# Optimization experiments

Measured on AMD Instinct MI355X. Metric: run time of the kernel, lower is better.

## Reference

```python
import jax, jax.numpy as jnp
import numpy as np

TAU = 0.05
EPS = 1e-12


def _l2_normalize(x):
    # F.normalize(p=2): x / max(||x||, eps)
    n = jnp.sqrt(jnp.sum(x * x, axis=-1, keepdims=True))
    return x / jnp.maximum(n, EPS)


def _masked_lse(sim, mask):
    # logsumexp over axis -1 restricted to mask; rows with empty mask are
    # masked out downstream (has_pos), so we guard the log to stay finite.
    neg_inf = jnp.finfo(sim.dtype).min
    mx = jnp.max(jnp.where(mask, sim, neg_inf), axis=-1)
    mx_safe = jnp.where(mx > neg_inf / 2, mx, 0.0)
    s = jnp.sum(jnp.where(mask, jnp.exp(sim - mx_safe[:, None]), 0.0), axis=-1)
    return mx_safe + jnp.log(jnp.where(s > 0, s, 1.0))


def setup_inputs() -> dict:
    key = jax.random.key(0)
    k1, k2, k3, k4 = jax.random.split(key, 4)
    B, S, D = 64, 128, 256
    return {
        "logits": jax.random.normal(k1, (B, S, D), dtype=jnp.float32),
        "labels": jax.random.normal(k2, (B, S, D), dtype=jnp.float32),
        "pad_mask": jax.random.randint(k3, (B, S), 0, 2, dtype=jnp.int32),
        "ad_idxs": jax.random.randint(k4, (B, S), 0, 500, dtype=jnp.int32),
    }


def reference(logits, labels, pad_mask, ad_idxs):
    B, S, D = logits.shape
    q = _l2_normalize(logits.reshape(B * S, D))
    k = _l2_normalize(labels.reshape(B * S, D))
    valid = pad_mask.reshape(B * S).astype(bool)
    ad = ad_idxs.reshape(B * S)

    sim = jnp.einsum("nd,md->nm", q, k) / TAU          # [N, N]
    pair_valid = valid[None, :] & valid[:, None]
    pos_mask = (ad[None, :] == ad[:, None]) & pair_valid

    pos_lse = _masked_lse(sim, pos_mask)
    all_lse = _masked_lse(sim, pair_valid)
    has_pos = jnp.any(pos_mask, axis=-1)

    loss_per_row = -(pos_lse - all_lse)
    # mean over rows with at least one positive (== loss_per_row[has_pos].mean())
    cnt = jnp.sum(has_pos.astype(sim.dtype))
    loss = jnp.sum(jnp.where(has_pos, loss_per_row, 0.0)) / jnp.maximum(cnt, 1.0)
    return loss
```

## Files before the change

kernel.cpp:

```cpp
#include <hip/hip_runtime.h>
#include <hip/hip_bf16.h>
#include <hip/hip_fp8.h>
#include <math.h>

typedef float f32x4 __attribute__((ext_vector_type(4)));
typedef int   i32x4 __attribute__((ext_vector_type(4)));
typedef int   v8i   __attribute__((ext_vector_type(8)));

constexpr int Nn = 8192;
constexpr int Dd = 256;
constexpr float LOG2E     = 1.4426950408889634f;
constexpr float SIM_SCALE = 20.0f * LOG2E;
constexpr float SIM_BIAS  = -20.0f * LOG2E;
constexpr int   SCALE1    = 0x7F7F7F7F;

typedef __attribute__((address_space(1))) const unsigned int gu32;
typedef __attribute__((address_space(3))) unsigned int lu32;
__device__ __forceinline__ void gload16(const unsigned char* g, unsigned char* l) {
  __builtin_amdgcn_global_load_lds((gu32*)(uintptr_t)g, (lu32*)(uintptr_t)l, 16, 0, 0);
}

__global__ __launch_bounds__(256) void prep_kernel(const float* __restrict__ logits,
                                                   const float* __restrict__ labels,
                                                   const int* __restrict__ pad,
                                                   unsigned char* __restrict__ qb,
                                                   unsigned char* __restrict__ kb,
                                                   float* __restrict__ cbias,
                                                   float* __restrict__ g_all,
                                                   float* __restrict__ g_pos) {
  const int j = blockIdx.x * 256 + threadIdx.x;
  if (j < Nn) {
    cbias[j] = pad[j] ? SIM_BIAS : -1e30f;
    g_all[j] = 0.0f;
    g_pos[j] = 0.0f;
  }

  const int gw   = (blockIdx.x * 256 + threadIdx.x) >> 6;
  const int lane = threadIdx.x & 63;
  const float* src;
  unsigned char* dst;
  int row;
  if (gw < Nn) { src = logits; dst = qb; row = gw; }
  else         { src = labels; dst = kb; row = gw - Nn; }

  const float4 v = *reinterpret_cast<const float4*>(src + (size_t)row * Dd + lane * 4);
  float ss = v.x * v.x + v.y * v.y + v.z * v.z + v.w * v.w;
#pragma unroll
  for (int m = 32; m >= 1; m >>= 1) ss += __shfl_xor(ss, m);
  const float scale = 1.0f / fmaxf(sqrtf(ss), 1e-12f);

  const __hip_fp8_e4m3 e0(v.x * scale);
  const __hip_fp8_e4m3 e1(v.y * scale);
  const __hip_fp8_e4m3 e2(v.z * scale);
  const __hip_fp8_e4m3 e3(v.w * scale);
  const unsigned int packed = (unsigned int)e0.__x |
                              ((unsigned int)e1.__x << 8) |
                              ((unsigned int)e2.__x << 16) |
                              ((unsigned int)e3.__x << 24);
  reinterpret_cast<unsigned int*>(dst + (size_t)row * Dd)[lane] = packed;
}

__global__ __launch_bounds__(256, 2) void gemm_lse_kernel(const unsigned char* __restrict__ qb,
                                                          const unsigned char* __restrict__ kb,
                                                          const float* __restrict__ cbias,
                                                          const int* __restrict__ ad,
                                                          float* __restrict__ g_all,
                                                          float* __restrict__ g_pos) {
  __shared__ unsigned char smem[65536];

  const int tid  = threadIdx.x;
  const int lane = tid & 63;
  const int w    = tid >> 6;
  const int wrow = (w >> 1) * 64;
  const int wcolL = (w & 1) * 64;
  const int lq   = lane & 15;
  const int qd   = lane >> 4;
  const int rowBase = blockIdx.x * 128;
  const int colBase = blockIdx.y * 1024;

  const int srl = lane >> 3;
  const int cg  = (lane & 7) ^ srl;
  const unsigned char* gA0 = qb + (size_t)(rowBase + w * 32 + srl) * Dd + cg * 16;
  const unsigned char* gB0 = kb + (size_t)(colBase + w * 32 + srl) * Dd + cg * 16;

#pragma unroll
  for (int kk = 0; kk < 2; ++kk)
#pragma unroll
    for (int i = 0; i < 4; ++i)
      gload16(gA0 + (size_t)i * 8 * Dd + kk * 128,
              &smem[kk * 16384 + (w * 32 + i * 8) * 128]);
#pragma unroll
  for (int i = 0; i < 4; ++i)
    gload16(gB0 + (size_t)i * 8 * Dd, &smem[32768 + (w * 32 + i * 8) * 128]);

  int rowAd[4][4];
#pragma unroll
  for (int mt = 0; mt < 4; ++mt)
#pragma unroll
    for (int r = 0; r < 4; ++r)
      rowAd[mt][r] = ad[rowBase + wrow + mt * 16 + qd * 4 + r];

  float apA[4][4], apP[4][4];
  f32x4 c[4][4];
#pragma unroll
  for (int mt = 0; mt < 4; ++mt)
#pragma unroll
    for (int r = 0; r < 4; ++r) {
      apA[mt][r] = 0.f;
      apP[mt][r] = 0.f;
      c[mt][r] = (f32x4){0.f, 0.f, 0.f, 0.f};
    }

  float colB[4];
  int colAd[4];

  __syncthreads();

  for (int t = 0; t < 16; ++t) {
    const int kk = t & 1;

    if (t + 1 < 16) {
      const int tn = t + 1;
      const unsigned char* g = gB0 + (size_t)((tn >> 1) * 128) * Dd + (tn & 1) * 128;
      unsigned char* dB = &smem[32768 + (tn & 1) * 16384 + (w * 32) * 128];
#pragma unroll
      for (int i = 0; i < 4; ++i)
        gload16(g + (size_t)i * 8 * Dd, dB + i * 8 * 128);
    }

    if (kk == 0) {
      const int ct = t >> 1;
#pragma unroll
      for (int nt = 0; nt < 4; ++nt) {
        const int col = colBase + ct * 128 + wcolL + nt * 16 + lq;
        colB[nt]  = cbias[col];
        colAd[nt] = ad[col];
      }
    }

    const int g0 = qd << 1;
    const unsigned char* Ah = &smem[kk * 16384];
    const unsigned char* Bh = &smem[32768 + (t & 1) * 16384];

    v8i af[4];
#pragma unroll
    for (int mt = 0; mt < 4; ++mt) {
      const int r = wrow + mt * 16 + lq;
      const i32x4 lo = *reinterpret_cast<const i32x4*>(&Ah[r * 128 + ((g0 ^ (r & 7)) << 4)]);
      const i32x4 hi = *reinterpret_cast<const i32x4*>(&Ah[r * 128 + (((g0 + 1) ^ (r & 7)) << 4)]);
      af[mt] = (v8i){lo.x, lo.y, lo.z, lo.w, hi.x, hi.y, hi.z, hi.w};
    }
#pragma unroll
    for (int nt = 0; nt < 4; ++nt) {
      const int r = wcolL + nt * 16 + lq;
      const i32x4 lo = *reinterpret_cast<const i32x4*>(&Bh[r * 128 + ((g0 ^ (r & 7)) << 4)]);
      const i32x4 hi = *reinterpret_cast<const i32x4*>(&Bh[r * 128 + (((g0 + 1) ^ (r & 7)) << 4)]);
      const v8i bfq = (v8i){lo.x, lo.y, lo.z, lo.w, hi.x, hi.y, hi.z, hi.w};
#pragma unroll
      for (int mt = 0; mt < 4; ++mt)
        c[mt][nt] = __builtin_amdgcn_mfma_scale_f32_16x16x128_f8f6f4(
            af[mt], bfq, c[mt][nt], 0, 0, 0, SCALE1, 0, SCALE1);
    }

    if (kk == 1) {
#pragma unroll
      for (int mt = 0; mt < 4; ++mt) {
#pragma unroll
        for (int r = 0; r < 4; ++r) {
          float a = 0.f, p = 0.f;
#pragma unroll
          for (int nt = 0; nt < 4; ++nt) {
            const float e = __builtin_amdgcn_exp2f(fmaf(c[mt][nt][r], SIM_SCALE, colB[nt]));
            a += e;
            p += (colAd[nt] == rowAd[mt][r]) ? e : 0.f;
          }
          apA[mt][r] += a;
          apP[mt][r] += p;
        }
      }
#pragma unroll
      for (int mt = 0; mt < 4; ++mt)
#pragma unroll
        for (int nt = 0; nt < 4; ++nt)
          c[mt][nt] = (f32x4){0.f, 0.f, 0.f, 0.f};
    }

    __syncthreads();
  }

#pragma unroll
  for (int mt = 0; mt < 4; ++mt) {
#pragma unroll
    for (int r = 0; r < 4; ++r) {
      float a = apA[mt][r], p = apP[mt][r];
#pragma unroll
      for (int m = 1; m < 16; m <<= 1) {
        a += __shfl_xor(a, m);
        p += __shfl_xor(p, m);
      }
      if (lq == 0) {
        const int row = rowBase + wrow + mt * 16 + qd * 4 + r;
        atomicAdd(&g_all[row], a);
        atomicAdd(&g_pos[row], p);
      }
    }
  }
}

__global__ __launch_bounds__(1024) void reduce_kernel(const float* __restrict__ g_all,
                                                      const float* __restrict__ g_pos,
                                                      const int* __restrict__ pad,
                                                      float* __restrict__ out) {
  __shared__ float sS[16], sC[16];
  const int t = threadIdx.x;
  float s = 0.f, c = 0.f;
  const float4* ga4 = (const float4*)g_all;
  const float4* gp4 = (const float4*)g_pos;
  const int4*   pd4 = (const int4*)pad;
  for (int i = t; i < Nn / 4; i += 1024) {
    const float4 ga = ga4[i];
    const float4 gp = gp4[i];
    const int4   pd = pd4[i];
    if (pd.x) { s += __logf(ga.x) - __logf(gp.x); c += 1.f; }
    if (pd.y) { s += __logf(ga.y) - __logf(gp.y); c += 1.f; }
    if (pd.z) { s += __logf(ga.z) - __logf(gp.z); c += 1.f; }
    if (pd.w) { s += __logf(ga.w) - __logf(gp.w); c += 1.f; }
  }
#pragma unroll
  for (int m = 32; m >= 1; m >>= 1) {
    s += __shfl_xor(s, m);
    c += __shfl_xor(c, m);
  }
  if ((t & 63) == 0) { sS[t >> 6] = s; sC[t >> 6] = c; }
  __syncthreads();
  if (t == 0) {
    float S = 0.f, C = 0.f;
#pragma unroll
    for (int i = 0; i < 16; ++i) { S += sS[i]; C += sC[i]; }
    out[0] = S / fmaxf(C, 1.0f);
  }
}

extern "C" void kernel_launch(void* const* d_in, const int* in_sizes, int n_in,
                              void* d_out, int out_size, void* d_ws, size_t ws_size,
                              hipStream_t stream) {
  const float* logits = (const float*)d_in[0];
  const float* labels = (const float*)d_in[1];
  const int*   pad    = (const int*)d_in[2];
  const int*   ad     = (const int*)d_in[3];

  char* ws = (char*)d_ws;
  unsigned char* qb = (unsigned char*)(ws);
  unsigned char* kb = (unsigned char*)(ws + 2097152);
  float*  cb   = (float*)(ws + 4194304);
  float*  gAll = (float*)(ws + 4227072);
  float*  gPos = (float*)(ws + 4259840);
  float*  out  = (float*)d_out;

  prep_kernel<<<4096, 256, 0, stream>>>(logits, labels, pad, qb, kb, cb, gAll, gPos);
  gemm_lse_kernel<<<dim3(64, 8), 256, 0, stream>>>(qb, kb, cb, ad, gAll, gPos);
  reduce_kernel<<<1, 1024, 0, stream>>>(gAll, gPos, pad, out);
}
```

Measured before the change: 104.2 us.

## Keep Q tile in registers, halve column tile and LDS for higher occupancy

Loads the full-depth A (query) fragments into registers once instead of re-reading them from LDS every step. The K tile is now staged as full 256-byte rows per phase, and each wave processes a 64-column block. Column span per block is halved and the grid doubled, which cuts LDS to 48KB and raises the occupancy hint to 3 blocks per CU. The trade-off is more blocks each reloading the same A tile, more atomics per row, and higher register pressure from holding A in registers.

```diff
diff --git a/kernel.cpp b/kernel.cpp
--- a/kernel.cpp
+++ b/kernel.cpp
@@ -60,38 +60,45 @@
   reinterpret_cast<unsigned int*>(dst + (size_t)row * Dd)[lane] = packed;
 }
 
-__global__ __launch_bounds__(256, 2) void gemm_lse_kernel(const unsigned char* __restrict__ qb,
+__global__ __launch_bounds__(256, 3) void gemm_lse_kernel(const unsigned char* __restrict__ qb,
                                                           const unsigned char* __restrict__ kb,
                                                           const float* __restrict__ cbias,
                                                           const int* __restrict__ ad,
                                                           float* __restrict__ g_all,
                                                           float* __restrict__ g_pos) {
-  __shared__ unsigned char smem[65536];
+  __shared__ unsigned char smem[49152];
 
   const int tid  = threadIdx.x;
   const int lane = tid & 63;
   const int w    = tid >> 6;
-  const int wrow = (w >> 1) * 64;
-  const int wcolL = (w & 1) * 64;
+  const int wrow  = (w >> 1) * 64;
+  const int wcolL = (w & 1) * 32;
   const int lq   = lane & 15;
   const int qd   = lane >> 4;
   const int rowBase = blockIdx.x * 128;
-  const int colBase = blockIdx.y * 1024;
+  const int colBase = blockIdx.y * 512;
 
   const int srl = lane >> 3;
   const int cg  = (lane & 7) ^ srl;
   const unsigned char* gA0 = qb + (size_t)(rowBase + w * 32 + srl) * Dd + cg * 16;
-  const unsigned char* gB0 = kb + (size_t)(colBase + w * 32 + srl) * Dd + cg * 16;
-
 #pragma unroll
   for (int kk = 0; kk < 2; ++kk)
 #pragma unroll
     for (int i = 0; i < 4; ++i)
       gload16(gA0 + (size_t)i * 8 * Dd + kk * 128,
               &smem[kk * 16384 + (w * 32 + i * 8) * 128]);
-#pragma unroll
-  for (int i = 0; i < 4; ++i)
-    gload16(gB0 + (size_t)i * 8 * Dd, &smem[32768 + (w * 32 + i * 8) * 128]);
+
+  const int rl = lane >> 4;
+  const int sg = lane & 15;
+  const unsigned char* gBe = kb + (size_t)(colBase + w * 16 + rl) * Dd + ((sg ^ rl) << 4);
+  const unsigned char* gBo = kb + (size_t)(colBase + w * 16 + rl) * Dd + ((sg ^ (4 + rl)) << 4);
+
+  {
+    unsigned char* dB = &smem[32768 + (w * 16) * 256];
+#pragma unroll
+    for (int i = 0; i < 4; ++i)
+      gload16((i & 1 ? gBo : gBe) + (size_t)i * 1024, dB + i * 1024);
+  }
 
   int rowAd[4][4];
 #pragma unroll
@@ -101,88 +108,90 @@
       rowAd[mt][r] = ad[rowBase + wrow + mt * 16 + qd * 4 + r];
 
   float apA[4][4], apP[4][4];
-  f32x4 c[4][4];
 #pragma unroll
   for (int mt = 0; mt < 4; ++mt)
 #pragma unroll
     for (int r = 0; r < 4; ++r) {
       apA[mt][r] = 0.f;
       apP[mt][r] = 0.f;
-      c[mt][r] = (f32x4){0.f, 0.f, 0.f, 0.f};
-    }
-
-  float colB[4];
-  int colAd[4];
+    }
 
   __syncthreads();
 
-  for (int t = 0; t < 16; ++t) {
-    const int kk = t & 1;
-
-    if (t + 1 < 16) {
-      const int tn = t + 1;
-      const unsigned char* g = gB0 + (size_t)((tn >> 1) * 128) * Dd + (tn & 1) * 128;
-      unsigned char* dB = &smem[32768 + (tn & 1) * 16384 + (w * 32) * 128];
+  const int sl = lq & 7;
+  const int s0 = ((qd * 2) ^ sl) << 4;
+  const int s1 = ((qd * 2 + 1) ^ sl) << 4;
+
+  v8i afReg[2][4];
+#pragma unroll
+  for (int kk = 0; kk < 2; ++kk) {
+    const unsigned char* Ah = &smem[kk * 16384];
+#pragma unroll
+    for (int mt = 0; mt < 4; ++mt) {
+      const int rb = (wrow + mt * 16 + lq) * 128;
+      i32x4* ph_ = reinterpret_cast<i32x4*>(&afReg[kk][mt]);
+      ph_[0] = *reinterpret_cast<const i32x4*>(&Ah[rb + s0]);
+      ph_[1] = *reinterpret_cast<const i32x4*>(&Ah[rb + s1]);
+    }
+  }
+
+  __syncthreads();
+
+  const f32x4 CZ = (f32x4){0.f, 0.f, 0.f, 0.f};
+
+  for (int ph = 0; ph < 8; ++ph) {
+    if (ph < 7) {
+      unsigned char* dB = &smem[(((ph + 1) & 1) ? 0u : 32768u) + (w * 16) * 256];
+      const size_t gOff = (size_t)(ph + 1) * 16384;
 #pragma unroll
       for (int i = 0; i < 4; ++i)
-        gload16(g + (size_t)i * 8 * Dd, dB + i * 8 * 128);
-    }
-
-    if (kk == 0) {
-      const int ct = t >> 1;
-#pragma unroll
-      for (int nt = 0; nt < 4; ++nt) {
-        const int col = colBase + ct * 128 + wcolL + nt * 16 + lq;
-        colB[nt]  = cbias[col];
-        colAd[nt] = ad[col];
-      }
-    }
-
-    const int g0 = qd << 1;
-    const unsigned char* Ah = &smem[kk * 16384];
-    const unsigned char* Bh = &smem[32768 + (t & 1) * 16384];
-
-    v8i af[4];
+        gload16((i & 1 ? gBo : gBe) + gOff + (size_t)i * 1024, dB + i * 1024);
+    }
+
+    float colB[2];
+    int colAd[2];
+#pragma unroll
+    for (int nt = 0; nt < 2; ++nt) {
+      const int col = colBase + ph * 64 + wcolL + nt * 16 + lq;
+      colB[nt]  = cbias[col];
+      colAd[nt] = ad[col];
+    }
+
+    const unsigned char* Bh = &smem[(ph & 1) ? 0u : 32768u];
+    f32x4 c[4][2];
+#pragma unroll
+    for (int nt = 0; nt < 2; ++nt) {
+      const int rb = (wcolL + nt * 16 + lq) * 256;
+      v8i bf0, bf1;
+      i32x4* p0 = reinterpret_cast<i32x4*>(&bf0);
+      p0[0] = *reinterpret_cast<const i32x4*>(&Bh[rb + s0]);
+      p0[1] = *reinterpret_cast<const i32x4*>(&Bh[rb + s1]);
+      i32x4* p1 = reinterpret_cast<i32x4*>(&bf1);
+      p1[0] = *reinterpret_cast<const i32x4*>(&Bh[rb + s0 + 128]);
+      p1[1] = *reinterpret_cast<const i32x4*>(&Bh[rb + s1 + 128]);
+#pragma unroll
+      for (int mt = 0; mt < 4; ++mt) {
+        const f32x4 t = __builtin_amdgcn_mfma_scale_f32_16x16x128_f8f6f4(
+            afReg[0][mt], bf0, CZ, 0, 0, 0, SCALE1, 0, SCALE1);
+        c[mt][nt] = __builtin_amdgcn_mfma_scale_f32_16x16x128_f8f6f4(
+            afReg[1][mt], bf1, t, 0, 0, 0, SCALE1, 0, SCALE1);
+      }
+    }
+
 #pragma unroll
     for (int mt = 0; mt < 4; ++mt) {
-      const int r = wrow + mt * 16 + lq;
-      const i32x4 lo = *reinterpret_cast<const i32x4*>(&Ah[r * 128 + ((g0 ^ (r & 7)) << 4)]);
-      const i32x4 hi = *reinterpret_cast<const i32x4*>(&Ah[r * 128 + (((g0 + 1) ^ (r & 7)) << 4)]);
-      af[mt] = (v8i){lo.x, lo.y, lo.z, lo.w, hi.x, hi.y, hi.z, hi.w};
-    }
-#pragma unroll
-    for (int nt = 0; nt < 4; ++nt) {
-      const int r = wcolL + nt * 16 + lq;
-      const i32x4 lo = *reinterpret_cast<const i32x4*>(&Bh[r * 128 + ((g0 ^ (r & 7)) << 4)]);
-      const i32x4 hi = *reinterpret_cast<const i32x4*>(&Bh[r * 128 + (((g0 + 1) ^ (r & 7)) << 4)]);
-      const v8i bfq = (v8i){lo.x, lo.y, lo.z, lo.w, hi.x, hi.y, hi.z, hi.w};
-#pragma unroll
-      for (int mt = 0; mt < 4; ++mt)
-        c[mt][nt] = __builtin_amdgcn_mfma_scale_f32_16x16x128_f8f6f4(
-            af[mt], bfq, c[mt][nt], 0, 0, 0, SCALE1, 0, SCALE1);
-    }
-
-    if (kk == 1) {
-#pragma unroll
-      for (int mt = 0; mt < 4; ++mt) {
-#pragma unroll
-        for (int r = 0; r < 4; ++r) {
-          float a = 0.f, p = 0.f;
-#pragma unroll
-          for (int nt = 0; nt < 4; ++nt) {
-            const float e = __builtin_amdgcn_exp2f(fmaf(c[mt][nt][r], SIM_SCALE, colB[nt]));
-            a += e;
-            p += (colAd[nt] == rowAd[mt][r]) ? e : 0.f;
-          }
-          apA[mt][r] += a;
-          apP[mt][r] += p;
+#pragma unroll
+      for (int r = 0; r < 4; ++r) {
+        float a = 0.f, p = 0.f;
+#pragma unroll
+        for (int nt = 0; nt < 2; ++nt) {
+          const float e = __builtin_amdgcn_exp2f(fmaf(c[mt][nt][r], SIM_SCALE, colB[nt]));
+          a += e;
+          p += (colAd[nt] == rowAd[mt][r]) ? e : 0.f;
         }
-      }
-#pragma unroll
-      for (int mt = 0; mt < 4; ++mt)
-#pragma unroll
-        for (int nt = 0; nt < 4; ++nt)
-          c[mt][nt] = (f32x4){0.f, 0.f, 0.f, 0.f};
+        apA[mt][r] += a;
+        apP[mt][r] += p;
+      }
     }
 
     __syncthreads();
@@ -258,6 +267,6 @@
   float*  out  = (float*)d_out;
 
   prep_kernel<<<4096, 256, 0, stream>>>(logits, labels, pad, qb, kb, cb, gAll, gPos);
-  gemm_lse_kernel<<<dim3(64, 8), 256, 0, stream>>>(qb, kb, cb, ad, gAll, gPos);
+  gemm_lse_kernel<<<dim3(64, 16), 256, 0, stream>>>(qb, kb, cb, ad, gAll, gPos);
   reduce_kernel<<<1, 1024, 0, stream>>>(gAll, gPos, pad, out);
 }
```

Result: slower. 144.9 us (+39.1%).

## Load GEMM operands directly from global into registers, drop LDS staging

Applied to the files above, without the earlier changes.

Removes the shared-memory double-buffered pipeline (global_load_lds plus swizzled LDS reads and per-step __syncthreads). Each wave now keeps its full A fragments in registers for the whole kernel and reads B fragments straight from global memory per column tile, running both K halves back to back. This removes LDS traffic and block barriers, but each B tile is now fetched separately by the two waves that share it, so the kernel leans on L2/L1 hits. Register pressure also rises from the persistent A fragments.

```diff
diff --git a/kernel.cpp b/kernel.cpp
--- a/kernel.cpp
+++ b/kernel.cpp
@@ -13,12 +13,6 @@
 constexpr float SIM_SCALE = 20.0f * LOG2E;
 constexpr float SIM_BIAS  = -20.0f * LOG2E;
 constexpr int   SCALE1    = 0x7F7F7F7F;
-
-typedef __attribute__((address_space(1))) const unsigned int gu32;
-typedef __attribute__((address_space(3))) unsigned int lu32;
-__device__ __forceinline__ void gload16(const unsigned char* g, unsigned char* l) {
-  __builtin_amdgcn_global_load_lds((gu32*)(uintptr_t)g, (lu32*)(uintptr_t)l, 16, 0, 0);
-}
 
 __global__ __launch_bounds__(256) void prep_kernel(const float* __restrict__ logits,
                                                    const float* __restrict__ labels,
@@ -66,32 +60,27 @@
                                                           const int* __restrict__ ad,
                                                           float* __restrict__ g_all,
                                                           float* __restrict__ g_pos) {
-  __shared__ unsigned char smem[65536];
-
   const int tid  = threadIdx.x;
   const int lane = tid & 63;
   const int w    = tid >> 6;
-  const int wrow = (w >> 1) * 64;
+  const int wrow  = (w >> 1) * 64;
   const int wcolL = (w & 1) * 64;
   const int lq   = lane & 15;
   const int qd   = lane >> 4;
   const int rowBase = blockIdx.x * 128;
   const int colBase = blockIdx.y * 1024;
 
-  const int srl = lane >> 3;
-  const int cg  = (lane & 7) ^ srl;
-  const unsigned char* gA0 = qb + (size_t)(rowBase + w * 32 + srl) * Dd + cg * 16;
-  const unsigned char* gB0 = kb + (size_t)(colBase + w * 32 + srl) * Dd + cg * 16;
-
+  const unsigned char* pA = qb + (size_t)(rowBase + wrow + lq) * Dd + qd * 32;
+  v8i afReg[2][4];
 #pragma unroll
   for (int kk = 0; kk < 2; ++kk)
 #pragma unroll
-    for (int i = 0; i < 4; ++i)
-      gload16(gA0 + (size_t)i * 8 * Dd + kk * 128,
-              &smem[kk * 16384 + (w * 32 + i * 8) * 128]);
-#pragma unroll
-  for (int i = 0; i < 4; ++i)
-    gload16(gB0 + (size_t)i * 8 * Dd, &smem[32768 + (w * 32 + i * 8) * 128]);
+    for (int mt = 0; mt < 4; ++mt) {
+      const unsigned char* a = pA + mt * 16 * Dd + kk * 128;
+      i32x4* ph_ = reinterpret_cast<i32x4*>(&afReg[kk][mt]);
+      ph_[0] = *reinterpret_cast<const i32x4*>(a);
+      ph_[1] = *reinterpret_cast<const i32x4*>(a + 16);
+    }
 
   int rowAd[4][4];
 #pragma unroll
@@ -101,91 +90,65 @@
       rowAd[mt][r] = ad[rowBase + wrow + mt * 16 + qd * 4 + r];
 
   float apA[4][4], apP[4][4];
-  f32x4 c[4][4];
 #pragma unroll
   for (int mt = 0; mt < 4; ++mt)
 #pragma unroll
     for (int r = 0; r < 4; ++r) {
       apA[mt][r] = 0.f;
       apP[mt][r] = 0.f;
-      c[mt][r] = (f32x4){0.f, 0.f, 0.f, 0.f};
-    }
-
-  float colB[4];
-  int colAd[4];
-
-  __syncthreads();
-
-  for (int t = 0; t < 16; ++t) {
-    const int kk = t & 1;
-
-    if (t + 1 < 16) {
-      const int tn = t + 1;
-      const unsigned char* g = gB0 + (size_t)((tn >> 1) * 128) * Dd + (tn & 1) * 128;
-      unsigned char* dB = &smem[32768 + (tn & 1) * 16384 + (w * 32) * 128];
-#pragma unroll
-      for (int i = 0; i < 4; ++i)
-        gload16(g + (size_t)i * 8 * Dd, dB + i * 8 * 128);
-    }
-
-    if (kk == 0) {
-      const int ct = t >> 1;
-#pragma unroll
-      for (int nt = 0; nt < 4; ++nt) {
-        const int col = colBase + ct * 128 + wcolL + nt * 16 + lq;
-        colB[nt]  = cbias[col];
-        colAd[nt] = ad[col];
-      }
-    }
-
-    const int g0 = qd << 1;
-    const unsigned char* Ah = &smem[kk * 16384];
-    const unsigned char* Bh = &smem[32768 + (t & 1) * 16384];
-
-    v8i af[4];
+    }
+
+  const unsigned char* pB = kb + (size_t)(colBase + wcolL + lq) * Dd + qd * 32;
+  const float* pCb = cbias + colBase + wcolL + lq;
+  const int*   pAd = ad    + colBase + wcolL + lq;
+  const f32x4 CZ = (f32x4){0.f, 0.f, 0.f, 0.f};
+
+  for (int ct = 0; ct < 8; ++ct) {
+    const int cOff = ct * 128;
+
+    float colB[4];
+    int colAd[4];
+#pragma unroll
+    for (int nt = 0; nt < 4; ++nt) {
+      colB[nt]  = pCb[cOff + nt * 16];
+      colAd[nt] = pAd[cOff + nt * 16];
+    }
+
+    f32x4 c[4][4];
+#pragma unroll
+    for (int nt = 0; nt < 4; ++nt) {
+      const unsigned char* b = pB + (size_t)(cOff + nt * 16) * Dd;
+      v8i bf0, bf1;
+      i32x4* p0 = reinterpret_cast<i32x4*>(&bf0);
+      p0[0] = *reinterpret_cast<const i32x4*>(b);
+      p0[1] = *reinterpret_cast<const i32x4*>(b + 16);
+      i32x4* p1 = reinterpret_cast<i32x4*>(&bf1);
+      p1[0] = *reinterpret_cast<const i32x4*>(b + 128);
+      p1[1] = *reinterpret_cast<const i32x4*>(b + 144);
+#pragma unroll
+      for (int mt = 0; mt < 4; ++mt) {
+        const f32x4 t0 = __builtin_amdgcn_mfma_scale_f32_16x16x128_f8f6f4(
+            afReg[0][mt], bf0, CZ, 0, 0, 0, SCALE1, 0, SCALE1);
+        c[mt][nt] = __builtin_amdgcn_mfma_scale_f32_16x16x128_f8f6f4(
+            afReg[1][mt], bf1, t0, 0, 0, 0, SCALE1, 0, SCALE1);
+      }
+    }
+
 #pragma unroll
     for (int mt = 0; mt < 4; ++mt) {
-      const int r = wrow + mt * 16 + lq;
-      const i32x4 lo = *reinterpret_cast<const i32x4*>(&Ah[r * 128 + ((g0 ^ (r & 7)) << 4)]);
-      const i32x4 hi = *reinterpret_cast<const i32x4*>(&Ah[r * 128 + (((g0 + 1) ^ (r & 7)) << 4)]);
-      af[mt] = (v8i){lo.x, lo.y, lo.z, lo.w, hi.x, hi.y, hi.z, hi.w};
-    }
-#pragma unroll
-    for (int nt = 0; nt < 4; ++nt) {
-      const int r = wcolL + nt * 16 + lq;
-      const i32x4 lo = *reinterpret_cast<const i32x4*>(&Bh[r * 128 + ((g0 ^ (r & 7)) << 4)]);
-      const i32x4 hi = *reinterpret_cast<const i32x4*>(&Bh[r * 128 + (((g0 + 1) ^ (r & 7)) << 4)]);
-      const v8i bfq = (v8i){lo.x, lo.y, lo.z, lo.w, hi.x, hi.y, hi.z, hi.w};
-#pragma unroll
-      for (int mt = 0; mt < 4; ++mt)
-        c[mt][nt] = __builtin_amdgcn_mfma_scale_f32_16x16x128_f8f6f4(
-            af[mt], bfq, c[mt][nt], 0, 0, 0, SCALE1, 0, SCALE1);
-    }
-
-    if (kk == 1) {
-#pragma unroll
-      for (int mt = 0; mt < 4; ++mt) {
-#pragma unroll
-        for (int r = 0; r < 4; ++r) {
-          float a = 0.f, p = 0.f;
-#pragma unroll
-          for (int nt = 0; nt < 4; ++nt) {
-            const float e = __builtin_amdgcn_exp2f(fmaf(c[mt][nt][r], SIM_SCALE, colB[nt]));
-            a += e;
-            p += (colAd[nt] == rowAd[mt][r]) ? e : 0.f;
-          }
-          apA[mt][r] += a;
-          apP[mt][r] += p;
+#pragma unroll
+      for (int r = 0; r < 4; ++r) {
+        float a = 0.f, p = 0.f;
+#pragma unroll
+        for (int nt = 0; nt < 4; ++nt) {
+          const float e = __builtin_amdgcn_exp2f(fmaf(c[mt][nt][r], SIM_SCALE, colB[nt]));
+          a += e;
+          p += (colAd[nt] == rowAd[mt][r]) ? e : 0.f;
         }
-      }
-#pragma unroll
-      for (int mt = 0; mt < 4; ++mt)
-#pragma unroll
-        for (int nt = 0; nt < 4; ++nt)
-          c[mt][nt] = (f32x4){0.f, 0.f, 0.f, 0.f};
-    }
-
-    __syncthreads();
+        apA[mt][r] += a;
+        apP[mt][r] += p;
+      }
+    }
   }
 
 #pragma unroll
```

Measured after the change: 118.6 us. 1.14x slower.
